# Kernel tuning notes

Measured on AMD Instinct MI355X. Metric: run time of the kernel, lower is better.

Reference implementation:

```python
import jax, jax.numpy as jnp
import numpy as np

K_TOP = 2        # experts_per_tok
E_MLP = 8        # num_mlp_experts


def setup_inputs() -> dict:
    key = jax.random.key(0)
    ks = jax.random.split(key, 6)
    B, T, C, H, E_ve, V = 2, 2048, 1024, 2048, 2, 32000
    return {
        "x": jax.random.normal(ks[0], (B, T, C), dtype=jnp.float32),
        "token_ids": jax.random.randint(ks[1], (B, T), 0, V, dtype=jnp.int32),
        "w_up": jax.random.normal(ks[2], (E_MLP, H, C), dtype=jnp.float32) * 0.02,
        "w_down": jax.random.normal(ks[3], (E_MLP, C, H), dtype=jnp.float32) * 0.02,
        "router_w": jax.random.normal(ks[4], (E_MLP + E_ve, C), dtype=jnp.float32) * 0.02,
        "router_bias": jnp.zeros((E_MLP + E_ve,), dtype=jnp.float32),
        "ve_tables": jax.random.normal(ks[5], (E_ve, V, C), dtype=jnp.float32) * 0.02,
    }


def reference(x, token_ids, w_up, w_down, router_w, router_bias, ve_tables):
    B, T, C = x.shape
    N = B * T
    E_total = router_w.shape[0]
    x_flat = x.reshape(N, C)

    # Sigmoid router with aux-loss-free bias (DeepSeekV3 style): select top-k on
    # biased scores, gate with unbiased sigmoid scores normalized over the top-k.
    scores = jax.nn.sigmoid(x_flat @ router_w.T)              # (N, E_total)
    _, top_idx = jax.lax.top_k(scores + router_bias, K_TOP)   # (N, k)
    top_w = jnp.take_along_axis(scores, top_idx, axis=1)      # (N, k)
    top_w = top_w / jnp.sum(top_w, axis=1, keepdims=True)

    rows = jnp.arange(N)[:, None]
    sparse_w = jnp.zeros((N, E_total), dtype=x.dtype).at[rows, top_idx].set(top_w)

    # Dense all-expert FFN (relu^2 activation), then mask by routing weights.
    hidden = jnp.einsum('nc,ehc->enh', x_flat, w_up)          # (E_mlp, N, H)
    hidden = jnp.square(jax.nn.relu(hidden))
    mlp_out = jnp.einsum('enh,ech->enc', hidden, w_down)      # (E_mlp, N, C)
    mlp_contrib = jnp.einsum('enc,ne->nc', mlp_out, sparse_w[:, :E_MLP])

    # VE experts: shared embedding lookups, (E_ve, N, C).
    ve_out = ve_tables[:, token_ids.reshape(N), :]
    ve_contrib = jnp.einsum('enc,ne->nc', ve_out, sparse_w[:, E_MLP:])

    return (mlp_contrib + ve_contrib).reshape(B, T, C)
```

## Files before the change

kernel.cpp:

```cpp
#include <hip/hip_runtime.h>
#include <hip/hip_bf16.h>
#include <stdint.h>

#define N_TOK 4096
#define C_DIM 1024
#define H_DIM 2048
#define V_DIM 32000
#define NE_MLP 8
#define NE_TOT 10

typedef __attribute__((ext_vector_type(8))) short bf16x8;
typedef __attribute__((ext_vector_type(4))) short bf16x4;
typedef __attribute__((ext_vector_type(4))) float f32x4;

#define BM 128
#define BN 128
#define BND 64
#define HKE 32
#define HALF_ELEMS (128 * 32)
#define HALF_B (64 * 32)

__device__ __forceinline__ void gload16(const void* g, void* l) {
    __builtin_amdgcn_global_load_lds(
        (const __attribute__((address_space(1))) void*)g,
        (__attribute__((address_space(3))) void*)l,
        16, 0, 0);
}

__device__ __forceinline__ unsigned short bf16bits(float v) {
    __hip_bfloat16 h = __float2bfloat16(v);
    return *reinterpret_cast<unsigned short*>(&h);
}

#define CVT_W (NE_MLP * H_DIM * C_DIM / 4)
__global__ void __launch_bounds__(256) cvt_kernel(
    const float* __restrict__ wu, const float* __restrict__ wd,
    __hip_bfloat16* __restrict__ wub, __hip_bfloat16* __restrict__ wdb)
{
    const int i = blockIdx.x * 256 + threadIdx.x;
    const float* src;
    __hip_bfloat16* dst;
    int j;
    if (i < CVT_W) { src = wu; dst = wub; j = i; }
    else           { src = wd; dst = wdb; j = i - CVT_W; }
    f32x4 v = reinterpret_cast<const f32x4*>(src)[j];
    bf16x4 b;
    b.x = (short)bf16bits(v.x); b.y = (short)bf16bits(v.y);
    b.z = (short)bf16bits(v.z); b.w = (short)bf16bits(v.w);
    reinterpret_cast<bf16x4*>(dst)[j] = b;
}

__global__ void __launch_bounds__(256) router_kernel(
    const float* __restrict__ x, const float* __restrict__ rw,
    const float* __restrict__ rb, const int* __restrict__ token_ids,
    const float* __restrict__ vt, __hip_bfloat16* __restrict__ xb,
    int* __restrict__ tok_list, float* __restrict__ wlist,
    int* __restrict__ cnt, float* __restrict__ out)
{
    const int lane = threadIdx.x & 63;
    const int n = blockIdx.x * 4 + (threadIdx.x >> 6);
    const f32x4* xr  = reinterpret_cast<const f32x4*>(x + (size_t)n * C_DIM);
    const f32x4* rw4 = reinterpret_cast<const f32x4*>(rw);
    bf16x4* xbr = reinterpret_cast<bf16x4*>(xb + (size_t)n * C_DIM);

    float acc[NE_TOT];
    #pragma unroll
    for (int e = 0; e < NE_TOT; ++e) acc[e] = 0.f;

    #pragma unroll
    for (int kk = 0; kk < C_DIM / 256; ++kk) {
        f32x4 xv = xr[kk * 64 + lane];
        bf16x4 xbv;
        xbv.x = (short)bf16bits(xv.x); xbv.y = (short)bf16bits(xv.y);
        xbv.z = (short)bf16bits(xv.z); xbv.w = (short)bf16bits(xv.w);
        xbr[kk * 64 + lane] = xbv;
        #pragma unroll
        for (int e = 0; e < NE_TOT; ++e) {
            f32x4 wv = rw4[e * (C_DIM / 4) + kk * 64 + lane];
            acc[e] += xv.x * wv.x + xv.y * wv.y + xv.z * wv.z + xv.w * wv.w;
        }
    }
    #pragma unroll
    for (int e = 0; e < NE_TOT; ++e) {
        for (int m = 32; m > 0; m >>= 1) acc[e] += __shfl_xor(acc[e], m, 64);
    }

    float wv0 = 0.f, wv1 = 0.f;
    if (lane == 0) {
        float s[NE_TOT], sb[NE_TOT];
        #pragma unroll
        for (int e = 0; e < NE_TOT; ++e) {
            s[e]  = 1.f / (1.f + expf(-acc[e]));
            sb[e] = s[e] + rb[e];
        }
        int i0 = 0;
        #pragma unroll
        for (int e = 1; e < NE_TOT; ++e) if (sb[e] > sb[i0]) i0 = e;
        int i1 = (i0 == 0) ? 1 : 0;
        #pragma unroll
        for (int e = 0; e < NE_TOT; ++e)
            if (e != i0 && sb[e] > sb[i1]) i1 = e;

        float w0 = s[i0], w1 = s[i1];
        float inv = 1.f / (w0 + w1);
        w0 *= inv; w1 *= inv;

        int   idx[2] = {i0, i1};
        float wt[2]  = {w0, w1};
        #pragma unroll
        for (int k = 0; k < 2; ++k) {
            if (idx[k] < NE_MLP) {
                int p = atomicAdd(&cnt[idx[k]], 1);
                tok_list[idx[k] * N_TOK + p] = n;
                wlist[idx[k] * N_TOK + p] = wt[k];
            } else {
                if (idx[k] == NE_MLP) wv0 = wt[k]; else wv1 = wt[k];
            }
        }
    }
    wv0 = __shfl(wv0, 0, 64);
    wv1 = __shfl(wv1, 0, 64);
    const int t = token_ids[n];
    const f32x4* v0 = reinterpret_cast<const f32x4*>(vt + (size_t)t * C_DIM);
    const f32x4* v1 = reinterpret_cast<const f32x4*>(vt + ((size_t)V_DIM + t) * C_DIM);
    f32x4* orow = reinterpret_cast<f32x4*>(out + (size_t)n * C_DIM);
    #pragma unroll
    for (int q = 0; q < 4; ++q) {
        const int c = q * 64 + lane;
        f32x4 v = {0.f, 0.f, 0.f, 0.f};
        if (wv0 != 0.f) v += wv0 * v0[c];
        if (wv1 != 0.f) v += wv1 * v1[c];
        orow[c] = v;
    }
}

__global__ void __launch_bounds__(256) up_kernel(
    const __hip_bfloat16* __restrict__ xb, const __hip_bfloat16* __restrict__ wub,
    const int* __restrict__ tok_list, const int* __restrict__ cnt,
    __hip_bfloat16* __restrict__ hidden)
{
    const int lid = (blockIdx.z * 32 + blockIdx.y) * 16 + blockIdx.x;
    const int s   = (lid & 7) * 512 + (lid >> 3);
    const int bx = s & 15, by = (s >> 4) & 31, bz = s >> 9;

    const int e = bz;
    const int count = cnt[e];
    const int m0 = by * BM;
    if (m0 >= count) return;
    const int n0 = bx * BN;

    __shared__ __hip_bfloat16 lA[2 * HALF_ELEMS];
    __shared__ __hip_bfloat16 lB[2 * HALF_ELEMS];

    const int tid  = threadIdx.x;
    const int lane = tid & 63;
    const int wv   = tid >> 6;
    const int wm = (wv >> 1) * 64;
    const int wn = (wv & 1) * 64;

    const __hip_bfloat16* ga[2];
    const __hip_bfloat16* gb[2];
    __hip_bfloat16* la[2];
    __hip_bfloat16* lb[2];
    const __hip_bfloat16* wB = wub + (size_t)e * H_DIM * C_DIM;
    #pragma unroll
    for (int t = 0; t < 2; ++t) {
        const int srow = (wv + 4 * t) * 16 + (lane >> 2);
        int r = m0 + srow;
        const int tok = tok_list[e * N_TOK + (r < count ? r : count - 1)];
        ga[t] = xb + (size_t)tok * C_DIM + (lane & 3) * 8;
        gb[t] = wB + (size_t)(n0 + srow) * C_DIM + (lane & 3) * 8;
        la[t] = lA + (wv + 4 * t) * 512;
        lb[t] = lB + (wv + 4 * t) * 512;
    }

    f32x4 acc[4][4];
    #pragma unroll
    for (int i = 0; i < 4; ++i)
        #pragma unroll
        for (int j = 0; j < 4; ++j)
            acc[i][j] = (f32x4){0.f, 0.f, 0.f, 0.f};

    const int fm  = lane & 15;
    const int fkb = (lane >> 4) * 8;

    for (int k0 = 0; k0 < C_DIM; k0 += 2 * HKE) {
        __syncthreads();
        #pragma unroll
        for (int h = 0; h < 2; ++h) {
            #pragma unroll
            for (int t = 0; t < 2; ++t) {
                gload16(ga[t] + h * HKE, la[t] + h * HALF_ELEMS);
                gload16(gb[t] + h * HKE, lb[t] + h * HALF_ELEMS);
            }
        }
        #pragma unroll
        for (int t = 0; t < 2; ++t) { ga[t] += 2 * HKE; gb[t] += 2 * HKE; }
        __syncthreads();
        #pragma unroll
        for (int h = 0; h < 2; ++h) {
            bf16x8 af[4], bfr[4];
            #pragma unroll
            for (int i = 0; i < 4; ++i) {
                af[i]  = *reinterpret_cast<const bf16x8*>(lA + h * HALF_ELEMS + (wm + i * 16 + fm) * HKE + fkb);
                bfr[i] = *reinterpret_cast<const bf16x8*>(lB + h * HALF_ELEMS + (wn + i * 16 + fm) * HKE + fkb);
            }
            #pragma unroll
            for (int i = 0; i < 4; ++i)
                #pragma unroll
                for (int j = 0; j < 4; ++j)
                    acc[i][j] = __builtin_amdgcn_mfma_f32_16x16x32_bf16(af[i], bfr[j], acc[i][j], 0, 0, 0);
        }
    }

    const int fr = (lane >> 4) * 4;
    #pragma unroll
    for (int i = 0; i < 4; ++i) {
        #pragma unroll
        for (int r = 0; r < 4; ++r) {
            const int gr = m0 + wm + i * 16 + fr + r;
            const bool ok = gr < count;
            unsigned int pk[4];
            #pragma unroll
            for (int j = 0; j < 4; ++j) {
                float v = acc[i][j][r];
                v = v > 0.f ? v * v : 0.f;
                unsigned short b = bf16bits(v);
                int other = __shfl_xor((int)b, 1, 64);
                pk[j] = (unsigned)b | ((unsigned)other << 16);
            }
            if (ok && !(lane & 1)) {
                __hip_bfloat16* hrow = hidden + (size_t)(e * N_TOK + gr) * H_DIM + n0 + wn + fm;
                #pragma unroll
                for (int j = 0; j < 4; ++j)
                    *reinterpret_cast<unsigned int*>(hrow + j * 16) = pk[j];
            }
        }
    }
}

__global__ void __launch_bounds__(256) down_kernel(
    const __hip_bfloat16* __restrict__ hidden, const __hip_bfloat16* __restrict__ wdb,
    const int* __restrict__ tok_list, const float* __restrict__ wlist,
    const int* __restrict__ cnt, float* __restrict__ out)
{
    const int lid = (blockIdx.z * 32 + blockIdx.y) * 16 + blockIdx.x;
    const int s   = (lid & 7) * 512 + (lid >> 3);
    const int bx = s & 15, by = (s >> 4) & 31, bz = s >> 9;

    const int e = bz;
    const int count = cnt[e];
    const int m0 = by * BM;
    if (m0 >= count) return;
    const int n0 = bx * BND;

    __shared__ __hip_bfloat16 lA[2 * HALF_ELEMS];
    __shared__ __hip_bfloat16 lB[2 * HALF_B];

    const int tid  = threadIdx.x;
    const int lane = tid & 63;
    const int wv   = tid >> 6;
    const int wm = (wv >> 1) * 64;
    const int wn = (wv & 1) * 32;

    const __hip_bfloat16* ga[2];
    __hip_bfloat16* la[2];
    #pragma unroll
    for (int t = 0; t < 2; ++t) {
        const int srow = (wv + 4 * t) * 16 + (lane >> 2);
        int r = m0 + srow;
        const int arow = e * N_TOK + (r < count ? r : count - 1);
        ga[t] = hidden + (size_t)arow * H_DIM + (lane & 3) * 8;
        la[t] = lA + (wv + 4 * t) * 512;
    }
    const int srowB = wv * 16 + (lane >> 2);
    const __hip_bfloat16* gb = wdb + (size_t)e * C_DIM * H_DIM
                             + (size_t)(n0 + srowB) * H_DIM + (lane & 3) * 8;
    __hip_bfloat16* lb = lB + wv * 512;

    f32x4 acc[4][2];
    #pragma unroll
    for (int i = 0; i < 4; ++i)
        #pragma unroll
        for (int j = 0; j < 2; ++j)
            acc[i][j] = (f32x4){0.f, 0.f, 0.f, 0.f};

    const int fm  = lane & 15;
    const int fkb = (lane >> 4) * 8;

    for (int k0 = 0; k0 < H_DIM; k0 += 2 * HKE) {
        __syncthreads();
        #pragma unroll
        for (int h = 0; h < 2; ++h) {
            #pragma unroll
            for (int t = 0; t < 2; ++t)
                gload16(ga[t] + h * HKE, la[t] + h * HALF_ELEMS);
            gload16(gb + h * HKE, lb + h * HALF_B);
        }
        #pragma unroll
        for (int t = 0; t < 2; ++t) ga[t] += 2 * HKE;
        gb += 2 * HKE;
        __syncthreads();
        #pragma unroll
        for (int h = 0; h < 2; ++h) {
            bf16x8 af[4], bfr[2];
            #pragma unroll
            for (int i = 0; i < 4; ++i)
                af[i]  = *reinterpret_cast<const bf16x8*>(lA + h * HALF_ELEMS + (wm + i * 16 + fm) * HKE + fkb);
            #pragma unroll
            for (int j = 0; j < 2; ++j)
                bfr[j] = *reinterpret_cast<const bf16x8*>(lB + h * HALF_B + (wn + j * 16 + fm) * HKE + fkb);
            #pragma unroll
            for (int i = 0; i < 4; ++i)
                #pragma unroll
                for (int j = 0; j < 2; ++j)
                    acc[i][j] = __builtin_amdgcn_mfma_f32_16x16x32_bf16(af[i], bfr[j], acc[i][j], 0, 0, 0);
        }
    }

    const int fr = (lane >> 4) * 4;
    #pragma unroll
    for (int i = 0; i < 4; ++i) {
        #pragma unroll
        for (int r = 0; r < 4; ++r) {
            const int gr = m0 + wm + i * 16 + fr + r;
            if (gr < count) {
                const int   tok = tok_list[e * N_TOK + gr];
                const float w   = wlist[e * N_TOK + gr];
                float* orow = out + (size_t)tok * C_DIM + n0 + wn + fm;
                #pragma unroll
                for (int j = 0; j < 2; ++j)
                    __hip_atomic_fetch_add(orow + j * 16, w * acc[i][j][r],
                                           __ATOMIC_RELAXED, __HIP_MEMORY_SCOPE_AGENT);
            }
        }
    }
}

extern "C" void kernel_launch(void* const* d_in, const int* in_sizes, int n_in,
                              void* d_out, int out_size, void* d_ws, size_t ws_size,
                              hipStream_t stream)
{
    const float* x         = (const float*)d_in[0];
    const int*   token_ids = (const int*)  d_in[1];
    const float* w_up      = (const float*)d_in[2];
    const float* w_down    = (const float*)d_in[3];
    const float* router_w  = (const float*)d_in[4];
    const float* router_b  = (const float*)d_in[5];
    const float* ve_tables = (const float*)d_in[6];
    float* out = (float*)d_out;

    char* ws = (char*)d_ws;
    size_t off = 0;
    __hip_bfloat16* hidden  = (__hip_bfloat16*)(ws + off); off += (size_t)NE_MLP * N_TOK * H_DIM * 2;
    __hip_bfloat16* xb      = (__hip_bfloat16*)(ws + off); off += (size_t)N_TOK * C_DIM * 2;
    __hip_bfloat16* wub     = (__hip_bfloat16*)(ws + off); off += (size_t)NE_MLP * H_DIM * C_DIM * 2;
    __hip_bfloat16* wdb     = (__hip_bfloat16*)(ws + off); off += (size_t)NE_MLP * C_DIM * H_DIM * 2;
    int*   tok_list = (int*)  (ws + off); off += (size_t)NE_MLP * N_TOK * 4;
    float* wlist    = (float*)(ws + off); off += (size_t)NE_MLP * N_TOK * 4;
    int*   cnt      = (int*)  (ws + off); off += 64;

    hipMemsetAsync(cnt, 0, NE_MLP * sizeof(int), stream);

    router_kernel<<<N_TOK / 4, 256, 0, stream>>>(x, router_w, router_b,
                                                 token_ids, ve_tables, xb,
                                                 tok_list, wlist, cnt, out);
    cvt_kernel<<<2 * CVT_W / 256, 256, 0, stream>>>(w_up, w_down, wub, wdb);
    up_kernel<<<dim3(H_DIM / BN, N_TOK / BM, NE_MLP), 256, 0, stream>>>(
        xb, wub, tok_list, cnt, hidden);
    down_kernel<<<dim3(C_DIM / BND, N_TOK / BM, NE_MLP), 256, 0, stream>>>(
        hidden, wdb, tok_list, wlist, cnt, out);
}
```

Baseline: 583.0 us.

## Fuse router, convert, up and down GEMMs into one cooperative persistent kernel

Replaces four separate launches with a single cooperative persistent kernel. It runs the router and weight conversion, then two grid-wide syncs separate the up and down expert GEMM phases. Tiles are scheduled compactly from prefix sums of the per-expert counts, so only populated M-blocks are visited instead of launching the full grid with early-exit blocks. This removes launch gaps and empty blocks, at the cost of grid-sync overhead, a capped grid size, and losing the previous XCD-aware block swizzle.

New measurement: 903.6 us. 1.55x slower.

```diff
diff --git a/kernel.cpp b/kernel.cpp
--- a/kernel.cpp
+++ b/kernel.cpp
@@ -1,6 +1,9 @@
 #include <hip/hip_runtime.h>
+#include <hip/hip_cooperative_groups.h>
 #include <hip/hip_bf16.h>
 #include <stdint.h>
+
+namespace cg = cooperative_groups;
 
 #define N_TOK 4096
 #define C_DIM 1024
@@ -19,6 +22,7 @@
 #define HKE 32
 #define HALF_ELEMS (128 * 32)
 #define HALF_B (64 * 32)
+#define CVT_W (NE_MLP * H_DIM * C_DIM / 4)
 
 __device__ __forceinline__ void gload16(const void* g, void* l) {
     __builtin_amdgcn_global_load_lds(
@@ -32,36 +36,31 @@
     return *reinterpret_cast<unsigned short*>(&h);
 }
 
-#define CVT_W (NE_MLP * H_DIM * C_DIM / 4)
-__global__ void __launch_bounds__(256) cvt_kernel(
-    const float* __restrict__ wu, const float* __restrict__ wd,
-    __hip_bfloat16* __restrict__ wub, __hip_bfloat16* __restrict__ wdb)
-{
-    const int i = blockIdx.x * 256 + threadIdx.x;
-    const float* src;
-    __hip_bfloat16* dst;
-    int j;
-    if (i < CVT_W) { src = wu; dst = wub; j = i; }
-    else           { src = wd; dst = wdb; j = i - CVT_W; }
-    f32x4 v = reinterpret_cast<const f32x4*>(src)[j];
-    bf16x4 b;
-    b.x = (short)bf16bits(v.x); b.y = (short)bf16bits(v.y);
-    b.z = (short)bf16bits(v.z); b.w = (short)bf16bits(v.w);
-    reinterpret_cast<bf16x4*>(dst)[j] = b;
-}
-
-__global__ void __launch_bounds__(256) router_kernel(
-    const float* __restrict__ x, const float* __restrict__ rw,
-    const float* __restrict__ rb, const int* __restrict__ token_ids,
-    const float* __restrict__ vt, __hip_bfloat16* __restrict__ xb,
-    int* __restrict__ tok_list, float* __restrict__ wlist,
-    int* __restrict__ cnt, float* __restrict__ out)
+struct MegaParams {
+    const float* x;
+    const int*   tok_ids;
+    const float* wu;
+    const float* wd;
+    const float* rw;
+    const float* rb;
+    const float* vt;
+    __hip_bfloat16* xb;
+    __hip_bfloat16* wub;
+    __hip_bfloat16* wdb;
+    int*   tok_list;
+    float* wlist;
+    int*   cnt;
+    __hip_bfloat16* hidden;
+    float* out;
+};
+
+__device__ __forceinline__ void router_quad(const MegaParams& p, int q)
 {
     const int lane = threadIdx.x & 63;
-    const int n = blockIdx.x * 4 + (threadIdx.x >> 6);
-    const f32x4* xr  = reinterpret_cast<const f32x4*>(x + (size_t)n * C_DIM);
-    const f32x4* rw4 = reinterpret_cast<const f32x4*>(rw);
-    bf16x4* xbr = reinterpret_cast<bf16x4*>(xb + (size_t)n * C_DIM);
+    const int n = q * 4 + (threadIdx.x >> 6);
+    const f32x4* xr  = reinterpret_cast<const f32x4*>(p.x + (size_t)n * C_DIM);
+    const f32x4* rw4 = reinterpret_cast<const f32x4*>(p.rw);
+    bf16x4* xbr = reinterpret_cast<bf16x4*>(p.xb + (size_t)n * C_DIM);
 
     float acc[NE_TOT];
     #pragma unroll
@@ -91,7 +90,7 @@
         #pragma unroll
         for (int e = 0; e < NE_TOT; ++e) {
             s[e]  = 1.f / (1.f + expf(-acc[e]));
-            sb[e] = s[e] + rb[e];
+            sb[e] = s[e] + p.rb[e];
         }
         int i0 = 0;
         #pragma unroll
@@ -110,9 +109,9 @@
         #pragma unroll
         for (int k = 0; k < 2; ++k) {
             if (idx[k] < NE_MLP) {
-                int p = atomicAdd(&cnt[idx[k]], 1);
-                tok_list[idx[k] * N_TOK + p] = n;
-                wlist[idx[k] * N_TOK + p] = wt[k];
+                int pidx = atomicAdd(&p.cnt[idx[k]], 1);
+                p.tok_list[idx[k] * N_TOK + pidx] = n;
+                p.wlist[idx[k] * N_TOK + pidx] = wt[k];
             } else {
                 if (idx[k] == NE_MLP) wv0 = wt[k]; else wv1 = wt[k];
             }
@@ -120,13 +119,13 @@
     }
     wv0 = __shfl(wv0, 0, 64);
     wv1 = __shfl(wv1, 0, 64);
-    const int t = token_ids[n];
-    const f32x4* v0 = reinterpret_cast<const f32x4*>(vt + (size_t)t * C_DIM);
-    const f32x4* v1 = reinterpret_cast<const f32x4*>(vt + ((size_t)V_DIM + t) * C_DIM);
-    f32x4* orow = reinterpret_cast<f32x4*>(out + (size_t)n * C_DIM);
-    #pragma unroll
-    for (int q = 0; q < 4; ++q) {
-        const int c = q * 64 + lane;
+    const int t = p.tok_ids[n];
+    const f32x4* v0 = reinterpret_cast<const f32x4*>(p.vt + (size_t)t * C_DIM);
+    const f32x4* v1 = reinterpret_cast<const f32x4*>(p.vt + ((size_t)V_DIM + t) * C_DIM);
+    f32x4* orow = reinterpret_cast<f32x4*>(p.out + (size_t)n * C_DIM);
+    #pragma unroll
+    for (int qq = 0; qq < 4; ++qq) {
+        const int c = qq * 64 + lane;
         f32x4 v = {0.f, 0.f, 0.f, 0.f};
         if (wv0 != 0.f) v += wv0 * v0[c];
         if (wv1 != 0.f) v += wv1 * v1[c];
@@ -134,24 +133,10 @@
     }
 }
 
-__global__ void __launch_bounds__(256) up_kernel(
-    const __hip_bfloat16* __restrict__ xb, const __hip_bfloat16* __restrict__ wub,
-    const int* __restrict__ tok_list, const int* __restrict__ cnt,
-    __hip_bfloat16* __restrict__ hidden)
+__device__ __forceinline__ void up_tile(
+    const MegaParams& p, int e, int count, int m0, int n0,
+    __hip_bfloat16* lA, __hip_bfloat16* lB)
 {
-    const int lid = (blockIdx.z * 32 + blockIdx.y) * 16 + blockIdx.x;
-    const int s   = (lid & 7) * 512 + (lid >> 3);
-    const int bx = s & 15, by = (s >> 4) & 31, bz = s >> 9;
-
-    const int e = bz;
-    const int count = cnt[e];
-    const int m0 = by * BM;
-    if (m0 >= count) return;
-    const int n0 = bx * BN;
-
-    __shared__ __hip_bfloat16 lA[2 * HALF_ELEMS];
-    __shared__ __hip_bfloat16 lB[2 * HALF_ELEMS];
-
     const int tid  = threadIdx.x;
     const int lane = tid & 63;
     const int wv   = tid >> 6;
@@ -162,13 +147,13 @@
     const __hip_bfloat16* gb[2];
     __hip_bfloat16* la[2];
     __hip_bfloat16* lb[2];
-    const __hip_bfloat16* wB = wub + (size_t)e * H_DIM * C_DIM;
+    const __hip_bfloat16* wB = p.wub + (size_t)e * H_DIM * C_DIM;
     #pragma unroll
     for (int t = 0; t < 2; ++t) {
         const int srow = (wv + 4 * t) * 16 + (lane >> 2);
         int r = m0 + srow;
-        const int tok = tok_list[e * N_TOK + (r < count ? r : count - 1)];
-        ga[t] = xb + (size_t)tok * C_DIM + (lane & 3) * 8;
+        const int tok = p.tok_list[e * N_TOK + (r < count ? r : count - 1)];
+        ga[t] = p.xb + (size_t)tok * C_DIM + (lane & 3) * 8;
         gb[t] = wB + (size_t)(n0 + srow) * C_DIM + (lane & 3) * 8;
         la[t] = lA + (wv + 4 * t) * 512;
         lb[t] = lB + (wv + 4 * t) * 512;
@@ -230,7 +215,7 @@
                 pk[j] = (unsigned)b | ((unsigned)other << 16);
             }
             if (ok && !(lane & 1)) {
-                __hip_bfloat16* hrow = hidden + (size_t)(e * N_TOK + gr) * H_DIM + n0 + wn + fm;
+                __hip_bfloat16* hrow = p.hidden + (size_t)(e * N_TOK + gr) * H_DIM + n0 + wn + fm;
                 #pragma unroll
                 for (int j = 0; j < 4; ++j)
                     *reinterpret_cast<unsigned int*>(hrow + j * 16) = pk[j];
@@ -239,24 +224,10 @@
     }
 }
 
-__global__ void __launch_bounds__(256) down_kernel(
-    const __hip_bfloat16* __restrict__ hidden, const __hip_bfloat16* __restrict__ wdb,
-    const int* __restrict__ tok_list, const float* __restrict__ wlist,
-    const int* __restrict__ cnt, float* __restrict__ out)
+__device__ __forceinline__ void down_tile(
+    const MegaParams& p, int e, int count, int m0, int n0,
+    __hip_bfloat16* lA, __hip_bfloat16* lB)
 {
-    const int lid = (blockIdx.z * 32 + blockIdx.y) * 16 + blockIdx.x;
-    const int s   = (lid & 7) * 512 + (lid >> 3);
-    const int bx = s & 15, by = (s >> 4) & 31, bz = s >> 9;
-
-    const int e = bz;
-    const int count = cnt[e];
-    const int m0 = by * BM;
-    if (m0 >= count) return;
-    const int n0 = bx * BND;
-
-    __shared__ __hip_bfloat16 lA[2 * HALF_ELEMS];
-    __shared__ __hip_bfloat16 lB[2 * HALF_B];
-
     const int tid  = threadIdx.x;
     const int lane = tid & 63;
     const int wv   = tid >> 6;
@@ -270,11 +241,11 @@
         const int srow = (wv + 4 * t) * 16 + (lane >> 2);
         int r = m0 + srow;
         const int arow = e * N_TOK + (r < count ? r : count - 1);
-        ga[t] = hidden + (size_t)arow * H_DIM + (lane & 3) * 8;
+        ga[t] = p.hidden + (size_t)arow * H_DIM + (lane & 3) * 8;
         la[t] = lA + (wv + 4 * t) * 512;
     }
     const int srowB = wv * 16 + (lane >> 2);
-    const __hip_bfloat16* gb = wdb + (size_t)e * C_DIM * H_DIM
+    const __hip_bfloat16* gb = p.wdb + (size_t)e * C_DIM * H_DIM
                              + (size_t)(n0 + srowB) * H_DIM + (lane & 3) * 8;
     __hip_bfloat16* lb = lB + wv * 512;
 
@@ -325,15 +296,70 @@
         for (int r = 0; r < 4; ++r) {
             const int gr = m0 + wm + i * 16 + fr + r;
             if (gr < count) {
-                const int   tok = tok_list[e * N_TOK + gr];
-                const float w   = wlist[e * N_TOK + gr];
-                float* orow = out + (size_t)tok * C_DIM + n0 + wn + fm;
+                const int   tok = p.tok_list[e * N_TOK + gr];
+                const float w   = p.wlist[e * N_TOK + gr];
+                float* orow = p.out + (size_t)tok * C_DIM + n0 + wn + fm;
                 #pragma unroll
                 for (int j = 0; j < 2; ++j)
                     __hip_atomic_fetch_add(orow + j * 16, w * acc[i][j][r],
                                            __ATOMIC_RELAXED, __HIP_MEMORY_SCOPE_AGENT);
             }
         }
+    }
+}
+
+__global__ void __launch_bounds__(256, 4) mega_kernel(MegaParams p)
+{
+    __shared__ __hip_bfloat16 lA[2 * HALF_ELEMS];
+    __shared__ __hip_bfloat16 lB[2 * HALF_ELEMS];
+
+    const int bid = blockIdx.x;
+    const int G   = gridDim.x;
+
+    for (int q = bid; q < N_TOK / 4; q += G)
+        router_quad(p, q);
+
+    for (int j = bid * 256 + (int)threadIdx.x; j < 2 * CVT_W; j += G * 256) {
+        const float* src;
+        __hip_bfloat16* dst;
+        int jj;
+        if (j < CVT_W) { src = p.wu; dst = p.wub; jj = j; }
+        else           { src = p.wd; dst = p.wdb; jj = j - CVT_W; }
+        f32x4 v = reinterpret_cast<const f32x4*>(src)[jj];
+        bf16x4 b;
+        b.x = (short)bf16bits(v.x); b.y = (short)bf16bits(v.y);
+        b.z = (short)bf16bits(v.z); b.w = (short)bf16bits(v.w);
+        reinterpret_cast<bf16x4*>(dst)[jj] = b;
+    }
+
+    __threadfence();
+    cg::this_grid().sync();
+
+    int cnts[NE_MLP];
+    int pre[NE_MLP + 1];
+    pre[0] = 0;
+    #pragma unroll
+    for (int e = 0; e < NE_MLP; ++e) {
+        cnts[e] = p.cnt[e];
+        pre[e + 1] = pre[e] + ((cnts[e] + BM - 1) >> 7);
+    }
+    const int nMB = pre[NE_MLP];
+
+    for (int t = bid; t < nMB * 16; t += G) {
+        const int em = t >> 4, nx = t & 15;
+        int e = 0;
+        while (em >= pre[e + 1]) ++e;
+        up_tile(p, e, cnts[e], (em - pre[e]) * BM, nx * BN, lA, lB);
+    }
+
+    __threadfence();
+    cg::this_grid().sync();
+
+    for (int t = bid; t < nMB * 16; t += G) {
+        const int em = t >> 4, nx = t & 15;
+        int e = 0;
+        while (em >= pre[e + 1]) ++e;
+        down_tile(p, e, cnts[e], (em - pre[e]) * BM, nx * BND, lA, lB);
     }
 }
 
@@ -362,12 +388,22 @@
 
     hipMemsetAsync(cnt, 0, NE_MLP * sizeof(int), stream);
 
-    router_kernel<<<N_TOK / 4, 256, 0, stream>>>(x, router_w, router_b,
-                                                 token_ids, ve_tables, xb,
-                                                 tok_list, wlist, cnt, out);
-    cvt_kernel<<<2 * CVT_W / 256, 256, 0, stream>>>(w_up, w_down, wub, wdb);
-    up_kernel<<<dim3(H_DIM / BN, N_TOK / BM, NE_MLP), 256, 0, stream>>>(
-        xb, wub, tok_list, cnt, hidden);
-    down_kernel<<<dim3(C_DIM / BND, N_TOK / BM, NE_MLP), 256, 0, stream>>>(
-        hidden, wdb, tok_list, wlist, cnt, out);
-}
+    MegaParams p;
+    p.x = x; p.tok_ids = token_ids; p.wu = w_up; p.wd = w_down;
+    p.rw = router_w; p.rb = router_b; p.vt = ve_tables;
+    p.xb = xb; p.wub = wub; p.wdb = wdb;
+    p.tok_list = tok_list; p.wlist = wlist; p.cnt = cnt;
+    p.hidden = hidden; p.out = out;
+
+    static int maxb = -1;
+    if (maxb < 0) {
+        hipOccupancyMaxActiveBlocksPerMultiprocessor(&maxb, mega_kernel, 256, 0);
+        if (maxb < 1) maxb = 1;
+    }
+    int grid = maxb * 256;
+    if (grid > 1024) grid = 1024;
+
+    void* kargs[] = { (void*)&p };
+    hipLaunchCooperativeKernel((void*)mega_kernel, dim3(grid), dim3(256),
+                               kargs, 0, stream);
+}
```
